# Kernel optimization log

Hardware: AMD Instinct MI355X
Metric: run time of the kernel (lower is better)

## Reference

```python
import jax, jax.numpy as jnp
import numpy as np

B, N, A, D = 1, 10000, 32, 256
H, DH = 4, 64


def setup_inputs() -> dict:
    key = jax.random.key(0)
    ks = jax.random.split(key, 9)
    x = jax.random.normal(ks[0], (B, N, D), dtype=jnp.float32)
    adj_kv_indices = jax.random.randint(ks[1], (B, N, A), 0, N, dtype=jnp.int64)
    mask = jax.random.randint(ks[2], (B, N, A), 0, 2) > 0
    Wq = jax.random.normal(ks[3], (D, H * DH), dtype=jnp.float32) * 0.02
    Wkv = jax.random.normal(ks[4], (D, 2 * H * DH), dtype=jnp.float32) * 0.02
    Wo = jax.random.normal(ks[5], (H * DH, D), dtype=jnp.float32) * 0.02
    bo = jnp.zeros((D,), dtype=jnp.float32)
    null_k = jax.random.normal(ks[6], (H, DH), dtype=jnp.float32)
    null_v = jax.random.normal(ks[7], (H, DH), dtype=jnp.float32)
    return {"x": x, "adj_kv_indices": adj_kv_indices, "mask": mask,
            "Wq": Wq, "Wkv": Wkv, "Wo": Wo, "bo": bo,
            "null_k": null_k, "null_v": null_v}


def reference(x, adj_kv_indices, mask, Wq, Wkv, Wo, bo, null_k, null_v):
    b, n, d = x.shape
    a = adj_kv_indices.shape[-1]
    h, dh = null_k.shape
    scale = dh ** -0.5

    # gather neighbor features: [b, n, a, d]
    kv_x = jnp.take_along_axis(x, adj_kv_indices.reshape(b, n * a)[:, :, None], axis=1)
    kv_x = kv_x.reshape(b, n, a, d)

    q = (x @ Wq).reshape(b, n, h, dh).transpose(0, 2, 1, 3)          # b h n dh
    kv = kv_x @ Wkv                                                   # b n a 2*h*dh
    k, v = jnp.split(kv, 2, axis=-1)
    k = k.reshape(b, n, a, h, dh).transpose(0, 3, 1, 2, 4)            # b h n a dh
    v = v.reshape(b, n, a, h, dh).transpose(0, 3, 1, 2, 4)

    # prepend null key/value token
    nk = jnp.broadcast_to(null_k[None, :, None, None, :], (b, h, n, 1, dh))
    nv = jnp.broadcast_to(null_v[None, :, None, None, :], (b, h, n, 1, dh))
    k = jnp.concatenate([nk, k], axis=-2)                             # b h n (a+1) dh
    v = jnp.concatenate([nv, v], axis=-2)

    full_mask = jnp.pad(mask, ((0, 0), (0, 0), (1, 0)), constant_values=True)
    full_mask = full_mask[:, None, :, :]                              # b 1 n (a+1)

    sim = jnp.einsum('bhnd,bhnad->bhna', q, k) * scale
    mask_value = -jnp.finfo(sim.dtype).max
    sim = jnp.where(full_mask, sim, mask_value)
    attn = jax.nn.softmax(sim, axis=-1)
    out = jnp.einsum('bhna,bhnad->bhnd', attn, v)
    out = out.transpose(0, 2, 1, 3).reshape(b, n, h * dh)
    return out @ Wo + bo
```

## Files before the change

kernel.cpp:

```cpp
#include <hip/hip_runtime.h>
#include <float.h>


typedef _Float16 f16;
typedef _Float16 f16x4 __attribute__((ext_vector_type(4)));
typedef _Float16 f16x8 __attribute__((ext_vector_type(8)));
typedef float    f32x4 __attribute__((ext_vector_type(4)));

#define GBM 64
#define GBN 64
#define GBK 32
#define LDK 40

__global__ __launch_bounds__(256) void cast_kernel(
    const float* __restrict__ in, f16* __restrict__ out, int n4)
{
    int i = blockIdx.x * 256 + threadIdx.x;
    if (i < n4) {
        float4 v = ((const float4*)in)[i];
        f16x4 o = {(f16)v.x, (f16)v.y, (f16)v.z, (f16)v.w};
        ((f16x4*)out)[i] = o;
    }
}

__global__ __launch_bounds__(256) void tcast_kernel(
    const float* __restrict__ W, f16* __restrict__ Wt, int K, int Nn, float mul)
{
    __shared__ float s[32][33];
    const int tx = threadIdx.x & 31, ty = threadIdx.x >> 5;
    const int kb = blockIdx.y * 32, nb = blockIdx.x * 32;
#pragma unroll
    for (int r = 0; r < 4; r++)
        s[ty + r * 8][tx] = W[(size_t)(kb + ty + r * 8) * Nn + nb + tx];
    __syncthreads();
#pragma unroll
    for (int r = 0; r < 4; r++)
        Wt[(size_t)(nb + ty + r * 8) * K + kb + tx] = (f16)(s[tx][ty + r * 8] * mul);
}

template <int OUT_HALF>
__global__ __launch_bounds__(256) void hgemm_kernel(
    const f16* __restrict__ A, const f16* __restrict__ Bt,
    void* __restrict__ C, const float* __restrict__ bias,
    int M, int Nn, int K)
{
    __shared__ f16 As[GBM][LDK];
    __shared__ f16 Bs[GBN][LDK];
    const int tid = threadIdx.x;
    const int w = tid >> 6;
    const int l = tid & 63;
    const int brow = blockIdx.y * GBM;
    const int bcol = blockIdx.x * GBN;

    const int sr = tid >> 2;
    const int sc = (tid & 3) * 8;

    const int arow = min(brow + sr, M - 1);
    const f16* aptr = A + (size_t)arow * K + sc;
    const f16* bptr = Bt + (size_t)(bcol + sr) * K + sc;

    const int fr = l & 15;
    const int k4 = (l >> 4) * 4;

    f32x4 acc[4];
#pragma unroll
    for (int c = 0; c < 4; c++) acc[c] = (f32x4){0.f, 0.f, 0.f, 0.f};

    for (int kk = 0; kk < K; kk += GBK) {
        *(f16x8*)&As[sr][sc] = *(const f16x8*)(aptr + kk);
        *(f16x8*)&Bs[sr][sc] = *(const f16x8*)(bptr + kk);
        __syncthreads();
#pragma unroll
        for (int k0 = 0; k0 < GBK; k0 += 16) {
            f16x4 af = *(const f16x4*)&As[w * 16 + fr][k0 + k4];
#pragma unroll
            for (int c = 0; c < 4; c++) {
                f16x4 bf = *(const f16x4*)&Bs[c * 16 + fr][k0 + k4];
                acc[c] = __builtin_amdgcn_mfma_f32_16x16x16f16(af, bf, acc[c], 0, 0, 0);
            }
        }
        __syncthreads();
    }

#pragma unroll
    for (int c = 0; c < 4; c++) {
        const int col = bcol + c * 16 + fr;
#pragma unroll
        for (int j = 0; j < 4; j++) {
            const int row = brow + w * 16 + (l >> 4) * 4 + j;
            if (row < M) {
                if (OUT_HALF)
                    ((f16*)C)[(size_t)row * Nn + col] = (f16)acc[c][j];
                else
                    ((float*)C)[(size_t)row * Nn + col] = acc[c][j] + bias[col];
            }
        }
    }
}

__global__ __launch_bounds__(256) void attn_kernel(
    const f16* __restrict__ Q, const f16* __restrict__ KV,
    const int* __restrict__ aidx, const int* __restrict__ amask,
    const float* __restrict__ nullk, const float* __restrict__ nullv,
    f16* __restrict__ out)
{
    const int n    = blockIdx.x;
    const int tid  = threadIdx.x;
    const int h    = tid >> 6;
    const int lane = tid & 63;
    const int g    = lane >> 4;
    const int gl   = lane & 15;

    __shared__ int sidx[32];
    __shared__ int smask[32];
    if (tid < 32) { sidx[tid] = aidx[n * 32 + tid]; smask[tid] = amask[n * 32 + tid]; }
    __syncthreads();

    f16x4 qh = *(const f16x4*)(Q + (size_t)n * 256 + h * 64 + gl * 4);
    const float q0 = (float)qh[0], q1 = (float)qh[1], q2 = (float)qh[2], q3 = (float)qh[3];

    float sim[9];
#pragma unroll
    for (int r = 0; r < 9; r++) sim[r] = -3.0e38f;

#pragma unroll
    for (int r = 0; r < 9; r++) {
        int a = r * 4 + g;
        if (a < 33) {
            bool doit = false;
            float k0, k1, k2, k3;
            if (a == 0) {
                doit = true;
                float4 k4 = ((const float4*)nullk)[h * 16 + gl];
                k0 = k4.x; k1 = k4.y; k2 = k4.z; k3 = k4.w;
            } else if (smask[a - 1] != 0) {
                doit = true;
                int j = sidx[a - 1];
                f16x4 kh = *(const f16x4*)(KV + (size_t)j * 512 + h * 64 + gl * 4);
                k0 = (float)kh[0]; k1 = (float)kh[1]; k2 = (float)kh[2]; k3 = (float)kh[3];
            }
            if (doit) {
                float s = q0 * k0 + q1 * k1 + q2 * k2 + q3 * k3;
                s += __shfl_xor(s, 1); s += __shfl_xor(s, 2);
                s += __shfl_xor(s, 4); s += __shfl_xor(s, 8);
                sim[r] = s;
            }
        }
    }

    float m = -3.0e38f;
#pragma unroll
    for (int r = 0; r < 9; r++) m = fmaxf(m, sim[r]);
    m = fmaxf(m, __shfl_xor(m, 16));
    m = fmaxf(m, __shfl_xor(m, 32));

    float p[9]; float l = 0.0f;
#pragma unroll
    for (int r = 0; r < 9; r++) {
        p[r] = (sim[r] > -1.0e37f) ? __expf(sim[r] - m) : 0.0f;
        l += p[r];
    }
    l += __shfl_xor(l, 16);
    l += __shfl_xor(l, 32);
    const float inv = 1.0f / l;
#pragma unroll
    for (int r = 0; r < 9; r++) p[r] *= inv;

    float acc = 0.0f;
    const float p0 = __shfl(p[0], 0);
    acc += p0 * nullv[h * 64 + lane];
#pragma unroll
    for (int a = 1; a <= 32; a++) {
        float pa = __shfl(p[a >> 2], (a & 3) << 4);
        if (pa != 0.0f) {
            int j = sidx[a - 1];
            acc += pa * (float)KV[(size_t)j * 512 + 256 + h * 64 + lane];
        }
    }
    out[(size_t)n * 256 + h * 64 + lane] = (f16)acc;
}

extern "C" void kernel_launch(void* const* d_in, const int* in_sizes, int n_in,
                              void* d_out, int out_size, void* d_ws, size_t ws_size,
                              hipStream_t stream)
{
    const float* x     = (const float*)d_in[0];
    const int*   aidx  = (const int*)  d_in[1];
    const int*   amask = (const int*)  d_in[2];
    const float* Wq    = (const float*)d_in[3];
    const float* Wkv   = (const float*)d_in[4];
    const float* Wo    = (const float*)d_in[5];
    const float* bo    = (const float*)d_in[6];
    const float* nk    = (const float*)d_in[7];
    const float* nv    = (const float*)d_in[8];
    float* out = (float*)d_out;

    const int N = 10000;
    f16* xh   = (f16*)d_ws;
    f16* Wqt  = xh   + (size_t)N * 256;
    f16* Wkvt = Wqt  + 256 * 256;
    f16* Wot  = Wkvt + 512 * 256;
    f16* Qh   = Wot  + 256 * 256;
    f16* KVh  = Qh   + (size_t)N * 256;
    f16* AOh  = KVh  + (size_t)N * 512;

    dim3 blk(256);
    cast_kernel<<<dim3((N * 256 / 4 + 255) / 256), blk, 0, stream>>>(x, xh, N * 256 / 4);
    tcast_kernel<<<dim3(8,  8), blk, 0, stream>>>(Wq,  Wqt,  256, 256, 0.125f);
    tcast_kernel<<<dim3(16, 8), blk, 0, stream>>>(Wkv, Wkvt, 256, 512, 1.0f);
    tcast_kernel<<<dim3(8,  8), blk, 0, stream>>>(Wo,  Wot,  256, 256, 1.0f);

    const int gm = (N + GBM - 1) / GBM;
    hgemm_kernel<1><<<dim3(4, gm), blk, 0, stream>>>(xh, Wqt,  Qh,  nullptr, N, 256, 256);
    hgemm_kernel<1><<<dim3(8, gm), blk, 0, stream>>>(xh, Wkvt, KVh, nullptr, N, 512, 256);
    attn_kernel   <<<dim3(N),      blk, 0, stream>>>(Qh, KVh, aidx, amask, nk, nv, AOh);
    hgemm_kernel<0><<<dim3(4, gm), blk, 0, stream>>>(AOh, Wot, out, bo,     N, 256, 256);
}
```

Baseline: 183.3 us.

## Fuse Q and KV projections, fold input cast into GEMM, enlarge tiles

Merges the separate Q and KV projection GEMMs into one GEMM over a concatenated 768-wide weight. The fp32-to-fp16 cast of x now happens inside the GEMM's A-tile load, so the standalone cast kernel goes away. The GEMM tile grows to 64x128x64, and the attention kernel reads from the interleaved QKV buffer. Attention also drops the per-neighbor mask branches in favour of unconditional loads with select, and shares probabilities through shared memory instead of shuffles. This trades fewer launches and less intermediate traffic for fewer GEMM blocks in the narrow output GEMM and extra loads of masked neighbors.

```diff
diff --git a/kernel.cpp b/kernel.cpp
--- a/kernel.cpp
+++ b/kernel.cpp
@@ -7,21 +7,10 @@
 typedef _Float16 f16x8 __attribute__((ext_vector_type(8)));
 typedef float    f32x4 __attribute__((ext_vector_type(4)));
 
-#define GBM 64
-#define GBN 64
-#define GBK 32
-#define LDK 40
-
-__global__ __launch_bounds__(256) void cast_kernel(
-    const float* __restrict__ in, f16* __restrict__ out, int n4)
-{
-    int i = blockIdx.x * 256 + threadIdx.x;
-    if (i < n4) {
-        float4 v = ((const float4*)in)[i];
-        f16x4 o = {(f16)v.x, (f16)v.y, (f16)v.z, (f16)v.w};
-        ((f16x4*)out)[i] = o;
-    }
-}
+#define BM 64
+#define BN 128
+#define BK 64
+#define LDK 72
 
 __global__ __launch_bounds__(256) void tcast_kernel(
     const float* __restrict__ W, f16* __restrict__ Wt, int K, int Nn, float mul)
@@ -38,43 +27,57 @@
         Wt[(size_t)(nb + ty + r * 8) * K + kb + tx] = (f16)(s[tx][ty + r * 8] * mul);
 }
 
-template <int OUT_HALF>
+template <int A_F32, int OUT_HALF>
 __global__ __launch_bounds__(256) void hgemm_kernel(
-    const f16* __restrict__ A, const f16* __restrict__ Bt,
+    const void* __restrict__ Av, const f16* __restrict__ Bt,
     void* __restrict__ C, const float* __restrict__ bias,
     int M, int Nn, int K)
 {
-    __shared__ f16 As[GBM][LDK];
-    __shared__ f16 Bs[GBN][LDK];
+    __shared__ f16 As[BM][LDK];
+    __shared__ f16 Bs[BN][LDK];
     const int tid = threadIdx.x;
     const int w = tid >> 6;
     const int l = tid & 63;
-    const int brow = blockIdx.y * GBM;
-    const int bcol = blockIdx.x * GBN;
-
-    const int sr = tid >> 2;
-    const int sc = (tid & 3) * 8;
-
-    const int arow = min(brow + sr, M - 1);
-    const f16* aptr = A + (size_t)arow * K + sc;
-    const f16* bptr = Bt + (size_t)(bcol + sr) * K + sc;
+    const int brow = blockIdx.y * BM;
+    const int bcol = blockIdx.x * BN;
+
+    const int sra = tid >> 2, sca = (tid & 3) * 16;
+    const int srb = tid >> 1, scb = (tid & 1) * 32;
+    const int arow = min(brow + sra, M - 1);
 
     const int fr = l & 15;
     const int k4 = (l >> 4) * 4;
 
-    f32x4 acc[4];
-#pragma unroll
-    for (int c = 0; c < 4; c++) acc[c] = (f32x4){0.f, 0.f, 0.f, 0.f};
-
-    for (int kk = 0; kk < K; kk += GBK) {
-        *(f16x8*)&As[sr][sc] = *(const f16x8*)(aptr + kk);
-        *(f16x8*)&Bs[sr][sc] = *(const f16x8*)(bptr + kk);
+    f32x4 acc[8];
+#pragma unroll
+    for (int c = 0; c < 8; c++) acc[c] = (f32x4){0.f, 0.f, 0.f, 0.f};
+
+    for (int kk = 0; kk < K; kk += BK) {
+        if (A_F32) {
+            const float* ap = (const float*)Av + (size_t)arow * K + kk + sca;
+#pragma unroll
+            for (int i = 0; i < 4; i++) {
+                float4 v = ((const float4*)ap)[i];
+                f16x4 o = {(f16)v.x, (f16)v.y, (f16)v.z, (f16)v.w};
+                *(f16x4*)&As[sra][sca + i * 4] = o;
+            }
+        } else {
+            const f16* ap = (const f16*)Av + (size_t)arow * K + kk + sca;
+            *(f16x8*)&As[sra][sca]     = *(const f16x8*)(ap);
+            *(f16x8*)&As[sra][sca + 8] = *(const f16x8*)(ap + 8);
+        }
+        {
+            const f16* bp = Bt + (size_t)(bcol + srb) * K + kk + scb;
+#pragma unroll
+            for (int i = 0; i < 4; i++)
+                *(f16x8*)&Bs[srb][scb + i * 8] = *(const f16x8*)(bp + i * 8);
+        }
         __syncthreads();
 #pragma unroll
-        for (int k0 = 0; k0 < GBK; k0 += 16) {
+        for (int k0 = 0; k0 < BK; k0 += 16) {
             f16x4 af = *(const f16x4*)&As[w * 16 + fr][k0 + k4];
 #pragma unroll
-            for (int c = 0; c < 4; c++) {
+            for (int c = 0; c < 8; c++) {
                 f16x4 bf = *(const f16x4*)&Bs[c * 16 + fr][k0 + k4];
                 acc[c] = __builtin_amdgcn_mfma_f32_16x16x16f16(af, bf, acc[c], 0, 0, 0);
             }
@@ -83,7 +86,7 @@
     }
 
 #pragma unroll
-    for (int c = 0; c < 4; c++) {
+    for (int c = 0; c < 8; c++) {
         const int col = bcol + c * 16 + fr;
 #pragma unroll
         for (int j = 0; j < 4; j++) {
@@ -99,58 +102,66 @@
 }
 
 __global__ __launch_bounds__(256) void attn_kernel(
-    const f16* __restrict__ Q, const f16* __restrict__ KV,
+    const f16* __restrict__ QKV,
     const int* __restrict__ aidx, const int* __restrict__ amask,
     const float* __restrict__ nullk, const float* __restrict__ nullv,
     f16* __restrict__ out)
 {
     const int n    = blockIdx.x;
     const int tid  = threadIdx.x;
-    const int h    = tid >> 6;
+    const int w    = tid >> 6;
+    const int h    = w;
     const int lane = tid & 63;
     const int g    = lane >> 4;
     const int gl   = lane & 15;
 
-    __shared__ int sidx[32];
-    __shared__ int smask[32];
-    if (tid < 32) { sidx[tid] = aidx[n * 32 + tid]; smask[tid] = amask[n * 32 + tid]; }
+    __shared__ int   sIdx[32];
+    __shared__ int   sMsk[32];
+    __shared__ float sP[4][33];
+
+    if (tid < 32) {
+        sIdx[tid] = aidx[n * 32 + tid];
+        sMsk[tid] = amask[n * 32 + tid];
+    }
     __syncthreads();
 
-    f16x4 qh = *(const f16x4*)(Q + (size_t)n * 256 + h * 64 + gl * 4);
+    f16x4 qh = *(const f16x4*)(QKV + (size_t)n * 768 + h * 64 + gl * 4);
     const float q0 = (float)qh[0], q1 = (float)qh[1], q2 = (float)qh[2], q3 = (float)qh[3];
 
     float sim[9];
-#pragma unroll
-    for (int r = 0; r < 9; r++) sim[r] = -3.0e38f;
-
-#pragma unroll
-    for (int r = 0; r < 9; r++) {
-        int a = r * 4 + g;
-        if (a < 33) {
-            bool doit = false;
-            float k0, k1, k2, k3;
-            if (a == 0) {
-                doit = true;
-                float4 k4 = ((const float4*)nullk)[h * 16 + gl];
-                k0 = k4.x; k1 = k4.y; k2 = k4.z; k3 = k4.w;
-            } else if (smask[a - 1] != 0) {
-                doit = true;
-                int j = sidx[a - 1];
-                f16x4 kh = *(const f16x4*)(KV + (size_t)j * 512 + h * 64 + gl * 4);
-                k0 = (float)kh[0]; k1 = (float)kh[1]; k2 = (float)kh[2]; k3 = (float)kh[3];
-            }
-            if (doit) {
-                float s = q0 * k0 + q1 * k1 + q2 * k2 + q3 * k3;
-                s += __shfl_xor(s, 1); s += __shfl_xor(s, 2);
-                s += __shfl_xor(s, 4); s += __shfl_xor(s, 8);
-                sim[r] = s;
-            }
-        }
-    }
-
-    float m = -3.0e38f;
-#pragma unroll
-    for (int r = 0; r < 9; r++) m = fmaxf(m, sim[r]);
+
+    {
+        float s;
+        if (g == 0) {
+            float4 nk4 = ((const float4*)nullk)[h * 16 + gl];
+            s = q0 * nk4.x + q1 * nk4.y + q2 * nk4.z + q3 * nk4.w;
+        } else {
+            int j = sIdx[g - 1];
+            f16x4 kh = *(const f16x4*)(QKV + (size_t)j * 768 + 256 + h * 64 + gl * 4);
+            s = q0 * (float)kh[0] + q1 * (float)kh[1] + q2 * (float)kh[2] + q3 * (float)kh[3];
+        }
+        s += __shfl_xor(s, 1); s += __shfl_xor(s, 2);
+        s += __shfl_xor(s, 4); s += __shfl_xor(s, 8);
+        bool ok = (g == 0) || (sMsk[g - 1] != 0);
+        sim[0] = ok ? s : -3.0e38f;
+    }
+
+#pragma unroll
+    for (int r = 1; r < 9; r++) {
+        int a  = r * 4 + g;
+        int ai = min(a - 1, 31);
+        int j  = sIdx[ai];
+        f16x4 kh = *(const f16x4*)(QKV + (size_t)j * 768 + 256 + h * 64 + gl * 4);
+        float s = q0 * (float)kh[0] + q1 * (float)kh[1] + q2 * (float)kh[2] + q3 * (float)kh[3];
+        s += __shfl_xor(s, 1); s += __shfl_xor(s, 2);
+        s += __shfl_xor(s, 4); s += __shfl_xor(s, 8);
+        bool ok = (a < 33) && (sMsk[ai] != 0);
+        sim[r] = ok ? s : -3.0e38f;
+    }
+
+    float m = sim[0];
+#pragma unroll
+    for (int r = 1; r < 9; r++) m = fmaxf(m, sim[r]);
     m = fmaxf(m, __shfl_xor(m, 16));
     m = fmaxf(m, __shfl_xor(m, 32));
 
@@ -163,19 +174,22 @@
     l += __shfl_xor(l, 16);
     l += __shfl_xor(l, 32);
     const float inv = 1.0f / l;
-#pragma unroll
-    for (int r = 0; r < 9; r++) p[r] *= inv;
-
-    float acc = 0.0f;
-    const float p0 = __shfl(p[0], 0);
-    acc += p0 * nullv[h * 64 + lane];
+
+    if (gl == 0) {
+#pragma unroll
+        for (int r = 0; r < 9; r++) {
+            int a = r * 4 + g;
+            if (a < 33) sP[w][a] = p[r] * inv;
+        }
+    }
+    __syncthreads();
+
+    float acc = sP[w][0] * nullv[h * 64 + lane];
 #pragma unroll
     for (int a = 1; a <= 32; a++) {
-        float pa = __shfl(p[a >> 2], (a & 3) << 4);
-        if (pa != 0.0f) {
-            int j = sidx[a - 1];
-            acc += pa * (float)KV[(size_t)j * 512 + 256 + h * 64 + lane];
-        }
+        int j = sIdx[a - 1];
+        float va = (float)QKV[(size_t)j * 768 + 512 + h * 64 + lane];
+        acc += sP[w][a] * va;
     }
     out[(size_t)n * 256 + h * 64 + lane] = (f16)acc;
 }
@@ -196,23 +210,18 @@
     float* out = (float*)d_out;
 
     const int N = 10000;
-    f16* xh   = (f16*)d_ws;
-    f16* Wqt  = xh   + (size_t)N * 256;
-    f16* Wkvt = Wqt  + 256 * 256;
-    f16* Wot  = Wkvt + 512 * 256;
-    f16* Qh   = Wot  + 256 * 256;
-    f16* KVh  = Qh   + (size_t)N * 256;
-    f16* AOh  = KVh  + (size_t)N * 512;
+    f16* Wqkvt = (f16*)d_ws;
+    f16* Wot   = Wqkvt + 768 * 256;
+    f16* QKV   = Wot   + 256 * 256;
+    f16* AOh   = QKV   + (size_t)N * 768;
 
     dim3 blk(256);
-    cast_kernel<<<dim3((N * 256 / 4 + 255) / 256), blk, 0, stream>>>(x, xh, N * 256 / 4);
-    tcast_kernel<<<dim3(8,  8), blk, 0, stream>>>(Wq,  Wqt,  256, 256, 0.125f);
-    tcast_kernel<<<dim3(16, 8), blk, 0, stream>>>(Wkv, Wkvt, 256, 512, 1.0f);
-    tcast_kernel<<<dim3(8,  8), blk, 0, stream>>>(Wo,  Wot,  256, 256, 1.0f);
-
-    const int gm = (N + GBM - 1) / GBM;
-    hgemm_kernel<1><<<dim3(4, gm), blk, 0, stream>>>(xh, Wqt,  Qh,  nullptr, N, 256, 256);
-    hgemm_kernel<1><<<dim3(8, gm), blk, 0, stream>>>(xh, Wkvt, KVh, nullptr, N, 512, 256);
-    attn_kernel   <<<dim3(N),      blk, 0, stream>>>(Qh, KVh, aidx, amask, nk, nv, AOh);
-    hgemm_kernel<0><<<dim3(4, gm), blk, 0, stream>>>(AOh, Wot, out, bo,     N, 256, 256);
-}
+    tcast_kernel<<<dim3(8,  8), blk, 0, stream>>>(Wq,  Wqkvt,             256, 256, 0.125f);
+    tcast_kernel<<<dim3(16, 8), blk, 0, stream>>>(Wkv, Wqkvt + 256 * 256, 256, 512, 1.0f);
+    tcast_kernel<<<dim3(8,  8), blk, 0, stream>>>(Wo,  Wot,               256, 256, 1.0f);
+
+    const int gm = (N + BM - 1) / BM;
+    hgemm_kernel<1, 1><<<dim3(768 / BN, gm), blk, 0, stream>>>(x,   Wqkvt, QKV, nullptr, N, 768, 256);
+    attn_kernel       <<<dim3(N),              blk, 0, stream>>>(QKV, aidx, amask, nk, nv, AOh);
+    hgemm_kernel<0, 0><<<dim3(256 / BN, gm), blk, 0, stream>>>(AOh, Wot,   out, bo,      N, 256, 256);
+}
```

Result: faster. 150.2 us (-18.1%).
